# Kernel tuning notes

Measured on AMD Instinct MI355X. Metric: run time of the kernel, lower is better.

The kernel has to match this reference:

```python
import jax, jax.numpy as jnp
import numpy as np

K_PERIODS = 4   # k_periods
PMAX = 64       # pmax
MIN_P = 16      # min_period_threshold (already clamped to <= PMAX)


def setup_inputs() -> dict:
    key = jax.random.key(0)
    B, T, N = 32, 512, 128
    x = jax.random.normal(key, (B, T, N), dtype=jnp.float32)
    return {"x": x}


def reference(x):
    # x: [B, T, N]
    B, T, N = x.shape
    K = K_PERIODS
    seqs = jnp.transpose(x, (0, 2, 1)).reshape(B * N, T)  # [BN, T]

    # top-k nonzero frequencies by rFFT amplitude
    spec = jnp.fft.rfft(seqs, axis=-1)                    # [BN, T//2+1]
    amp = jnp.abs(spec)
    amp = amp.at[..., 0].set(0.0)                         # zero DC component
    kamp, kidx = jax.lax.top_k(amp, K)                    # [BN, K] each
    kidx = jnp.maximum(kidx, 1)

    # periods and cycle counts
    P = jnp.clip(T // kidx, MIN_P, PMAX)                  # [BN, K]
    cycles = jnp.maximum(T // P, 1)                       # [BN, K]
    take = cycles * P

    # static upper bound on cycles (torch uses data-dependent cycles.max();
    # extra trailing cycle slots here are fully masked to zero)
    Cmax = T // MIN_P
    idx_c = jnp.arange(Cmax)                              # [Cmax]
    idx_p = jnp.arange(PMAX)                              # [Pmax]

    base = jnp.maximum(T - take, 0)[..., None, None]      # [BN, K, 1, 1]
    indices = base + idx_c[None, None, :, None] * P[..., None, None] \
              + idx_p[None, None, None, :]                # [BN, K, Cmax, Pmax]
    indices = jnp.clip(indices, 0, T - 1)

    # gather: broadcast seqs over (K, Cmax)
    gathered = jnp.take_along_axis(seqs[:, None, None, :], indices, axis=-1)

    mask = ((idx_c[None, None, :, None] < cycles[..., None, None]) &
            (idx_p[None, None, None, :] < P[..., None, None])).astype(x.dtype)
    gathered = gathered * mask

    gathered = gathered.reshape(B, N, K, Cmax, PMAX)
    mask = mask.reshape(B, N, K, Cmax, PMAX)
    kamp = kamp.reshape(B, N, K)
    return gathered, mask, kamp
```

## Files before the change

### kernel.cpp

```cpp
#include <hip/hip_runtime.h>
#include <math.h>

#define TLEN 512
#define NCH  128
#define KP   4
#define PMAXV 64
#define CMAXV 32
#define MINP 16
#define NSEQ 4096
#define OUTG ((size_t)NSEQ * KP * CMAXV * PMAXV)

__global__ __launch_bounds__(256) void periodicity_kernel(
    const float* __restrict__ x,
    float* __restrict__ out_g,
    float* __restrict__ out_m,
    float* __restrict__ out_a)
{
    const int s    = blockIdx.x;
    const int tid  = threadIdx.x;
    const int lane = tid & 63;
    const int wave = tid >> 6;

    __shared__ float   seqf[TLEN];
    __shared__ double2 X[TLEN];
    __shared__ double2 W[TLEN / 2];
    __shared__ double  amp[TLEN / 2 + 1];
    __shared__ double  bestv[KP];
    __shared__ int     besti[KP];
    __shared__ int     Ps[KP], Cs[KP], Bs[KP];

    const int b = s >> 7;
    const int n = s & (NCH - 1);
    const float* col = x + (size_t)b * TLEN * NCH + n;
    for (int i = tid; i < TLEN; i += 256)
        seqf[i] = col[(size_t)i * NCH];
    {
        double ang = -6.283185307179586476925286766559 * (double)tid / (double)TLEN;
        double sv, cv;
        sincos(ang, &sv, &cv);
        W[tid] = make_double2(cv, sv);
    }
    __syncthreads();

    {
        const int base = wave << 7;
        int i0 = base + lane, i1 = base + 64 + lane;
        int r0 = (int)(__brev((unsigned)i0) >> 23);
        int r1 = (int)(__brev((unsigned)i1) >> 23);
        X[i0] = make_double2((double)seqf[r0], 0.0);
        X[i1] = make_double2((double)seqf[r1], 0.0);
    }
    __builtin_amdgcn_wave_barrier();

    #pragma unroll
    for (int st = 1; st <= 7; ++st) {
        const int half = 1 << (st - 1);
        const int pos  = tid & (half - 1);
        const int i1   = ((tid >> (st - 1)) << st) + pos;
        const int i2   = i1 + half;
        const double2 wv = W[pos << (9 - st)];
        const double2 a  = X[i1];
        const double2 c  = X[i2];
        const double tr = wv.x * c.x - wv.y * c.y;
        const double ti = wv.x * c.y + wv.y * c.x;
        X[i1] = make_double2(a.x + tr, a.y + ti);
        X[i2] = make_double2(a.x - tr, a.y - ti);
        __builtin_amdgcn_wave_barrier();
    }

    #pragma unroll
    for (int st = 8; st <= 9; ++st) {
        __syncthreads();
        const int half = 1 << (st - 1);
        const int pos  = tid & (half - 1);
        const int i1   = ((tid >> (st - 1)) << st) + pos;
        const int i2   = i1 + half;
        const double2 wv = W[pos << (9 - st)];
        const double2 a  = X[i1];
        const double2 c  = X[i2];
        const double tr = wv.x * c.x - wv.y * c.y;
        const double ti = wv.x * c.y + wv.y * c.x;
        X[i1] = make_double2(a.x + tr, a.y + ti);
        X[i2] = make_double2(a.x - tr, a.y - ti);
    }
    __syncthreads();

    {
        double2 v = X[tid];
        amp[tid] = (tid == 0) ? 0.0 : sqrt(v.x * v.x + v.y * v.y);
        if (tid == 0) {
            double2 vn = X[TLEN / 2];
            amp[TLEN / 2] = sqrt(vn.x * vn.x + vn.y * vn.y);
        }
    }
    __syncthreads();

    if (wave == 0) {
        for (int q = 0; q < KP; ++q) {
            double v  = amp[lane];
            int    vi = lane;
            #pragma unroll
            for (int j = 1; j < 4; ++j) {
                double u = amp[lane + 64 * j];
                if (u > v) { v = u; vi = lane + 64 * j; }
            }
            if (lane == 0) {
                double u = amp[256];
                if (u > v) { v = u; vi = 256; }
            }
            #pragma unroll
            for (int off = 32; off > 0; off >>= 1) {
                double ov = __shfl_xor(v, off, 64);
                int    oi = __shfl_xor(vi, off, 64);
                if (ov > v || (ov == v && oi < vi)) { v = ov; vi = oi; }
            }
            if (lane == 0) {
                bestv[q] = v;
                besti[q] = vi;
                amp[vi] = -1.0;
            }
            __builtin_amdgcn_wave_barrier();
        }
        if (lane < KP) {
            int ki = besti[lane];
            if (ki < 1) ki = 1;
            int P = TLEN / ki;
            P = P < MINP ? MINP : (P > PMAXV ? PMAXV : P);
            int cyc = TLEN / P;
            Ps[lane] = P;
            Cs[lane] = cyc;
            Bs[lane] = TLEN - cyc * P;
            out_a[(size_t)s * KP + lane] = (float)bestv[lane];
        }
    }
    __syncthreads();

    float* og = out_g + (size_t)s * (KP * CMAXV * PMAXV);
    float* om = out_m + (size_t)s * (KP * CMAXV * PMAXV);
    const int pp = (tid & 15) << 2;
    for (int r = tid >> 4; r < KP * CMAXV; r += 16) {
        const int k = r >> 5;
        const int c = r & (CMAXV - 1);
        const int P = Ps[k], cyc = Cs[k], base = Bs[k];
        float4 g = make_float4(0.f, 0.f, 0.f, 0.f);
        float4 m = make_float4(0.f, 0.f, 0.f, 0.f);
        if (c < cyc) {
            const int idx = base + c * P + pp;
            if (pp     < P) { g.x = seqf[idx];     m.x = 1.f; }
            if (pp + 1 < P) { g.y = seqf[idx + 1]; m.y = 1.f; }
            if (pp + 2 < P) { g.z = seqf[idx + 2]; m.z = 1.f; }
            if (pp + 3 < P) { g.w = seqf[idx + 3]; m.w = 1.f; }
        }
        *(float4*)(og + r * PMAXV + pp) = g;
        *(float4*)(om + r * PMAXV + pp) = m;
    }
}

extern "C" void kernel_launch(void* const* d_in, const int* in_sizes, int n_in,
                              void* d_out, int out_size, void* d_ws, size_t ws_size,
                              hipStream_t stream) {
    const float* x = (const float*)d_in[0];
    float* out = (float*)d_out;
    float* og = out;
    float* om = out + OUTG;
    float* oa = om + OUTG;
    periodicity_kernel<<<dim3(NSEQ), dim3(256), 0, stream>>>(x, og, om, oa);
}
```

Before: 277.4 us.

## Precompute twiddles, pad LDS, drop sqrt in top-k, use nontemporal stores

Twiddle factors are computed once by a small setup kernel into workspace and loaded per block, replacing a per-block double-precision sincos. LDS arrays are padded every 16 elements to cut bank conflicts in the FFT butterflies. Top-k now ranks squared magnitudes and takes sqrt only for the four winners. Output stores become nontemporal float4 writes. The extra launch and the workspace dependency add a little overhead, and ranking on squared values could in rare cases order near-ties differently.

```diff
diff --git a/kernel.cpp b/kernel.cpp
--- a/kernel.cpp
+++ b/kernel.cpp
@@ -10,8 +10,21 @@
 #define NSEQ 4096
 #define OUTG ((size_t)NSEQ * KP * CMAXV * PMAXV)
 
+#define PAD(i) ((i) + ((i) >> 4))
+
+typedef float nfloat4 __attribute__((ext_vector_type(4)));
+
+__global__ void twiddle_setup(double2* __restrict__ Wg) {
+    const int j = threadIdx.x;
+    double ang = -6.283185307179586476925286766559 * (double)j / (double)TLEN;
+    double sv, cv;
+    sincos(ang, &sv, &cv);
+    Wg[j] = make_double2(cv, sv);
+}
+
 __global__ __launch_bounds__(256) void periodicity_kernel(
     const float* __restrict__ x,
+    const double2* __restrict__ Wg,
     float* __restrict__ out_g,
     float* __restrict__ out_m,
     float* __restrict__ out_a)
@@ -22,9 +35,9 @@
     const int wave = tid >> 6;
 
     __shared__ float   seqf[TLEN];
-    __shared__ double2 X[TLEN];
-    __shared__ double2 W[TLEN / 2];
-    __shared__ double  amp[TLEN / 2 + 1];
+    __shared__ double2 X[TLEN + (TLEN >> 4)];
+    __shared__ double2 W[256 + 16];
+    __shared__ double  amp2[280];
     __shared__ double  bestv[KP];
     __shared__ int     besti[KP];
     __shared__ int     Ps[KP], Cs[KP], Bs[KP];
@@ -35,10 +48,8 @@
     for (int i = tid; i < TLEN; i += 256)
         seqf[i] = col[(size_t)i * NCH];
     {
-        double ang = -6.283185307179586476925286766559 * (double)tid / (double)TLEN;
-        double sv, cv;
-        sincos(ang, &sv, &cv);
-        W[tid] = make_double2(cv, sv);
+        double2 w = Wg[tid];
+        W[PAD(tid)] = w;
     }
     __syncthreads();
 
@@ -47,8 +58,8 @@
         int i0 = base + lane, i1 = base + 64 + lane;
         int r0 = (int)(__brev((unsigned)i0) >> 23);
         int r1 = (int)(__brev((unsigned)i1) >> 23);
-        X[i0] = make_double2((double)seqf[r0], 0.0);
-        X[i1] = make_double2((double)seqf[r1], 0.0);
+        X[PAD(i0)] = make_double2((double)seqf[r0], 0.0);
+        X[PAD(i1)] = make_double2((double)seqf[r1], 0.0);
     }
     __builtin_amdgcn_wave_barrier();
 
@@ -58,13 +69,13 @@
         const int pos  = tid & (half - 1);
         const int i1   = ((tid >> (st - 1)) << st) + pos;
         const int i2   = i1 + half;
-        const double2 wv = W[pos << (9 - st)];
-        const double2 a  = X[i1];
-        const double2 c  = X[i2];
+        const double2 wv = W[PAD(pos << (9 - st))];
+        const double2 a  = X[PAD(i1)];
+        const double2 c  = X[PAD(i2)];
         const double tr = wv.x * c.x - wv.y * c.y;
         const double ti = wv.x * c.y + wv.y * c.x;
-        X[i1] = make_double2(a.x + tr, a.y + ti);
-        X[i2] = make_double2(a.x - tr, a.y - ti);
+        X[PAD(i1)] = make_double2(a.x + tr, a.y + ti);
+        X[PAD(i2)] = make_double2(a.x - tr, a.y - ti);
         __builtin_amdgcn_wave_barrier();
     }
 
@@ -75,37 +86,37 @@
         const int pos  = tid & (half - 1);
         const int i1   = ((tid >> (st - 1)) << st) + pos;
         const int i2   = i1 + half;
-        const double2 wv = W[pos << (9 - st)];
-        const double2 a  = X[i1];
-        const double2 c  = X[i2];
+        const double2 wv = W[PAD(pos << (9 - st))];
+        const double2 a  = X[PAD(i1)];
+        const double2 c  = X[PAD(i2)];
         const double tr = wv.x * c.x - wv.y * c.y;
         const double ti = wv.x * c.y + wv.y * c.x;
-        X[i1] = make_double2(a.x + tr, a.y + ti);
-        X[i2] = make_double2(a.x - tr, a.y - ti);
+        X[PAD(i1)] = make_double2(a.x + tr, a.y + ti);
+        X[PAD(i2)] = make_double2(a.x - tr, a.y - ti);
     }
     __syncthreads();
 
     {
-        double2 v = X[tid];
-        amp[tid] = (tid == 0) ? 0.0 : sqrt(v.x * v.x + v.y * v.y);
+        double2 v = X[PAD(tid)];
+        amp2[PAD(tid)] = (tid == 0) ? 0.0 : (v.x * v.x + v.y * v.y);
         if (tid == 0) {
-            double2 vn = X[TLEN / 2];
-            amp[TLEN / 2] = sqrt(vn.x * vn.x + vn.y * vn.y);
+            double2 vn = X[PAD(TLEN / 2)];
+            amp2[PAD(TLEN / 2)] = vn.x * vn.x + vn.y * vn.y;
         }
     }
     __syncthreads();
 
     if (wave == 0) {
         for (int q = 0; q < KP; ++q) {
-            double v  = amp[lane];
+            double v  = amp2[PAD(lane)];
             int    vi = lane;
             #pragma unroll
             for (int j = 1; j < 4; ++j) {
-                double u = amp[lane + 64 * j];
+                double u = amp2[PAD(lane + 64 * j)];
                 if (u > v) { v = u; vi = lane + 64 * j; }
             }
             if (lane == 0) {
-                double u = amp[256];
+                double u = amp2[PAD(256)];
                 if (u > v) { v = u; vi = 256; }
             }
             #pragma unroll
@@ -117,7 +128,7 @@
             if (lane == 0) {
                 bestv[q] = v;
                 besti[q] = vi;
-                amp[vi] = -1.0;
+                amp2[PAD(vi)] = -1.0;
             }
             __builtin_amdgcn_wave_barrier();
         }
@@ -130,7 +141,7 @@
             Ps[lane] = P;
             Cs[lane] = cyc;
             Bs[lane] = TLEN - cyc * P;
-            out_a[(size_t)s * KP + lane] = (float)bestv[lane];
+            out_a[(size_t)s * KP + lane] = (float)sqrt(bestv[lane]);
         }
     }
     __syncthreads();
@@ -142,8 +153,8 @@
         const int k = r >> 5;
         const int c = r & (CMAXV - 1);
         const int P = Ps[k], cyc = Cs[k], base = Bs[k];
-        float4 g = make_float4(0.f, 0.f, 0.f, 0.f);
-        float4 m = make_float4(0.f, 0.f, 0.f, 0.f);
+        nfloat4 g = (nfloat4)(0.f, 0.f, 0.f, 0.f);
+        nfloat4 m = (nfloat4)(0.f, 0.f, 0.f, 0.f);
         if (c < cyc) {
             const int idx = base + c * P + pp;
             if (pp     < P) { g.x = seqf[idx];     m.x = 1.f; }
@@ -151,8 +162,8 @@
             if (pp + 2 < P) { g.z = seqf[idx + 2]; m.z = 1.f; }
             if (pp + 3 < P) { g.w = seqf[idx + 3]; m.w = 1.f; }
         }
-        *(float4*)(og + r * PMAXV + pp) = g;
-        *(float4*)(om + r * PMAXV + pp) = m;
+        __builtin_nontemporal_store(g, (nfloat4*)(og + r * PMAXV + pp));
+        __builtin_nontemporal_store(m, (nfloat4*)(om + r * PMAXV + pp));
     }
 }
 
@@ -164,5 +175,8 @@
     float* og = out;
     float* om = out + OUTG;
     float* oa = om + OUTG;
-    periodicity_kernel<<<dim3(NSEQ), dim3(256), 0, stream>>>(x, og, om, oa);
+    double2* Wg = (double2*)d_ws;
+
+    twiddle_setup<<<dim3(1), dim3(256), 0, stream>>>(Wg);
+    periodicity_kernel<<<dim3(NSEQ), dim3(256), 0, stream>>>(x, Wg, og, om, oa);
 }
```

New measurement: 287.9 us. 3.8% more time.
